# Kernel tuning notes

Hardware: AMD Instinct MI355X
Metric: run time of the kernel (lower is better)

Reference implementation:

```python
import jax, jax.numpy as jnp
import numpy as np


def setup_inputs() -> dict:
    key = jax.random.key(0)
    ks = jax.random.split(key, 10)
    B, T = 256, 256
    num_q, dk, dv, C = 1000, 128, 128, 32
    xn_k = (2.0 / (dk + C)) ** 0.5   # xavier_normal for Mk
    xn_v = (2.0 / (C + dv)) ** 0.5   # xavier_normal for Mv
    return dict(
        skills=jax.random.randint(ks[0], (B, T), 0, num_q),
        responses=jax.random.randint(ks[1], (B, T), 0, 2),
        k_emb=jax.random.normal(ks[2], (num_q, dk), dtype=jnp.float32) * 0.05,
        v_emb=jax.random.normal(ks[3], (2 * num_q, dv), dtype=jnp.float32) * 0.05,
        Mk=jax.random.normal(ks[4], (dk, C), dtype=jnp.float32) * xn_k,
        Mv0=jax.random.normal(ks[5], (C, dv), dtype=jnp.float32) * xn_v,
        f_W=jax.random.normal(ks[6], (2 * dk, dk), dtype=jnp.float32) * 0.05,
        f_b=jnp.zeros((dk,), jnp.float32),
        p_W=jax.random.normal(ks[7], (dk, 1), dtype=jnp.float32) * 0.05,
        p_b=jnp.zeros((1,), jnp.float32),
        e_W=jax.random.normal(ks[8], (dv, dv), dtype=jnp.float32) * 0.05,
        e_b=jnp.zeros((dv,), jnp.float32),
        a_W=jax.random.normal(ks[9], (dv, dv), dtype=jnp.float32) * 0.05,
        a_b=jnp.zeros((dv,), jnp.float32),
    )


def reference(skills, responses, k_emb, v_emb, Mk, Mv0, f_W, f_b,
              p_W, p_b, e_W, e_b, a_W, a_b):
    num_q = k_emb.shape[0]
    B = skills.shape[0]
    masked_r = responses * (responses > -1).astype(responses.dtype)
    qr = skills + num_q * masked_r
    kt_all = k_emb[skills]   # (B, T, dk)
    vt_all = v_emb[qr]       # (B, T, dv)
    Mvt0 = jnp.broadcast_to(Mv0[None], (B,) + Mv0.shape)  # (B, C, dv)

    def step(Mvt, xs):
        kt, vt = xs                                      # (B,dk), (B,dv)
        wt = jax.nn.softmax(kt @ Mk, axis=-1)            # (B, C) read weights
        rt = jnp.einsum('bc,bcd->bd', wt, Mvt)           # memory read
        ft = jnp.tanh(jnp.concatenate([rt, kt], axis=-1) @ f_W + f_b)
        pt = jax.nn.sigmoid(ft @ p_W + p_b)[:, 0]        # (B,)
        et = jax.nn.sigmoid(vt @ e_W + e_b)              # erase gate
        at = jnp.tanh(vt @ a_W + a_b)                    # add vector
        Mvt = Mvt * (1.0 - wt[:, :, None] * et[:, None, :]) \
              + wt[:, :, None] * at[:, None, :]
        return Mvt, pt

    xs = (jnp.swapaxes(kt_all, 0, 1), jnp.swapaxes(vt_all, 0, 1))  # time-major
    _, p = jax.lax.scan(step, Mvt0, xs)                  # (T, B)
    p = jnp.swapaxes(p, 0, 1)                            # (B, T)
    pred = p[:, :-1]
    true = responses[:, 1:].astype(jnp.float32)
    return pred, true
```

## Files before the change

kernel.cpp:

```cpp
#include <hip/hip_runtime.h>
#include <math.h>

#define BB 256
#define TT 256
#define NQ 1000
#define DK 128
#define DV 128
#define CC 32

typedef short s16x8 __attribute__((ext_vector_type(8)));
typedef float f32x4 __attribute__((ext_vector_type(4)));
typedef float f32x2 __attribute__((ext_vector_type(2)));

__device__ __forceinline__ float fast_sigmoid(float x) {
    x = fminf(fmaxf(x, -30.f), 30.f);
    return 1.f / (1.f + __expf(-x));
}
__device__ __forceinline__ float fast_tanh(float x) {
    x = fminf(fmaxf(x, -15.f), 15.f);
    float t = __expf(2.f * x);
    return (t - 1.f) / (t + 1.f);
}
__device__ __forceinline__ unsigned short f2bf(float f) {
    unsigned u = __float_as_uint(f);
    u += 0x7fffu + ((u >> 16) & 1u);
    return (unsigned short)(u >> 16);
}
__device__ __forceinline__ float bf2f(unsigned short h) {
    return __uint_as_float((unsigned)h << 16);
}
__device__ __forceinline__ unsigned u4get(uint4 v, int i) {
    return i == 0 ? v.x : i == 1 ? v.y : i == 2 ? v.z : v.w;
}
__device__ __forceinline__ f32x2 mk2(float x, float y) { f32x2 r; r.x = x; r.y = y; return r; }
__device__ __forceinline__ f32x2 fma2(f32x2 a, f32x2 b, f32x2 c) {
    return __builtin_elementwise_fma(a, b, c);
}
__device__ __forceinline__ s16x8 cvt8(float4 v0, float4 v1) {
    s16x8 f;
    f[0] = (short)f2bf(v0.x); f[1] = (short)f2bf(v0.y);
    f[2] = (short)f2bf(v0.z); f[3] = (short)f2bf(v0.w);
    f[4] = (short)f2bf(v1.x); f[5] = (short)f2bf(v1.y);
    f[6] = (short)f2bf(v1.z); f[7] = (short)f2bf(v1.w);
    return f;
}

__global__ __launch_bounds__(256) void conv_kernel(
    const float* __restrict__ eW, const float* __restrict__ aW,
    const float* __restrict__ fW, const float* __restrict__ Mk,
    unsigned short* __restrict__ eWt, unsigned short* __restrict__ aWt,
    unsigned short* __restrict__ fWat, unsigned short* __restrict__ fWbt,
    unsigned short* __restrict__ Mkt)
{
    int idx = blockIdx.x * 256 + threadIdx.x;
    if (idx < 16384) {
        int n = idx >> 7, k = idx & 127;
        eWt[idx] = f2bf(eW[k * 128 + n]);
    } else if (idx < 32768) {
        int i = idx - 16384; int n = i >> 7, k = i & 127;
        aWt[i] = f2bf(aW[k * 128 + n]);
    } else if (idx < 49152) {
        int i = idx - 32768; int n = i >> 7, k = i & 127;
        fWat[i] = f2bf(fW[k * 128 + n]);
    } else if (idx < 65536) {
        int i = idx - 49152; int n = i >> 7, k = i & 127;
        fWbt[i] = f2bf(fW[(128 + k) * 128 + n]);
    } else if (idx < 69632) {
        int i = idx - 65536; int n = i >> 7, k = i & 127;
        Mkt[i] = f2bf(Mk[k * 32 + n]);
    }
}

__global__ __launch_bounds__(256) void pre_kernel(
    const int* __restrict__ skills, const int* __restrict__ responses,
    const float* __restrict__ k_emb, const float* __restrict__ v_emb,
    const float* __restrict__ fb, const float* __restrict__ eb,
    const float* __restrict__ ab,
    const unsigned short* __restrict__ Mkt, const unsigned short* __restrict__ fWbt,
    const unsigned short* __restrict__ eWt, const unsigned short* __restrict__ aWt,
    float* __restrict__ Wo, unsigned* __restrict__ EA,
    unsigned short* __restrict__ Ko, float* __restrict__ outTrue,
    int t0, int Tc)
{
    const int tid = threadIdx.x;
    const int lane = tid & 63;
    const int m_base = (tid >> 6) * 16;
    const int mrow = lane & 15, quad = lane >> 4;
    const size_t base = (size_t)blockIdx.x * 64;

    __shared__ __align__(16) unsigned short Wlds[128 * 136];

    int grow = (int)base + m_base + mrow;
    int gb = grow / Tc;
    int gt = t0 + (grow - gb * Tc);
    int gi = gb * TT + gt;
    int s = skills[gi];
    int r = responses[gi];
    int q = s + NQ * ((r > -1) ? r : 0);
    if (quad == 0 && gt >= 1) outTrue[gb * (TT - 1) + (gt - 1)] = (float)r;

    {
        int n = tid >> 3, k0 = (tid & 7) * 16;
        *(s16x8*)&Wlds[n * 136 + k0]     = *(const s16x8*)&Mkt[n * 128 + k0];
        *(s16x8*)&Wlds[n * 136 + k0 + 8] = *(const s16x8*)&Mkt[n * 128 + k0 + 8];
    }

    s16x8 aF[4];
    {
        const float* kr = k_emb + (size_t)s * DK + quad * 8;
#pragma unroll
        for (int kb = 0; kb < 4; ++kb)
            aF[kb] = cvt8(*(const float4*)(kr + kb * 32),
                          *(const float4*)(kr + kb * 32 + 4));
    }
    __syncthreads();

    {
        f32x4 l0 = {0.f, 0.f, 0.f, 0.f}, l1 = {0.f, 0.f, 0.f, 0.f};
#pragma unroll
        for (int kb = 0; kb < 4; ++kb) {
            s16x8 b0 = *(const s16x8*)&Wlds[mrow * 136 + kb * 32 + quad * 8];
            s16x8 b1 = *(const s16x8*)&Wlds[(16 + mrow) * 136 + kb * 32 + quad * 8];
            l0 = __builtin_amdgcn_mfma_f32_16x16x32_bf16(aF[kb], b0, l0, 0, 0, 0);
            l1 = __builtin_amdgcn_mfma_f32_16x16x32_bf16(aF[kb], b1, l1, 0, 0, 0);
        }
#pragma unroll
        for (int reg = 0; reg < 4; ++reg) {
            float a0 = l0[reg], a1 = l1[reg];
            float m = fmaxf(a0, a1);
#pragma unroll
            for (int off = 1; off < 16; off <<= 1)
                m = fmaxf(m, __shfl_xor(m, off, 64));
            float e0 = __expf(a0 - m), e1 = __expf(a1 - m);
            float ssum = e0 + e1;
#pragma unroll
            for (int off = 1; off < 16; off <<= 1)
                ssum += __shfl_xor(ssum, off, 64);
            float inv = 1.f / ssum;
            size_t rowg = base + m_base + quad * 4 + reg;
            Wo[rowg * 32 + mrow]      = e0 * inv;
            Wo[rowg * 32 + 16 + mrow] = e1 * inv;
        }
    }
    __syncthreads();

    {
        int n = tid >> 1, k0 = (tid & 1) * 64;
#pragma unroll
        for (int j = 0; j < 8; ++j)
            *(s16x8*)&Wlds[n * 136 + k0 + j * 8] = *(const s16x8*)&fWbt[n * 128 + k0 + j * 8];
    }
    __syncthreads();

    s16x8 vF[4];
    {
        const float* vr = v_emb + (size_t)q * DV + quad * 8;
#pragma unroll
        for (int kb = 0; kb < 4; ++kb)
            vF[kb] = cvt8(*(const float4*)(vr + kb * 32),
                          *(const float4*)(vr + kb * 32 + 4));
    }

#pragma unroll
    for (int nt = 0; nt < 8; ++nt) {
        f32x4 acc = {0.f, 0.f, 0.f, 0.f};
#pragma unroll
        for (int kb = 0; kb < 4; ++kb) {
            s16x8 bf = *(const s16x8*)&Wlds[(nt * 16 + mrow) * 136 + kb * 32 + quad * 8];
            acc = __builtin_amdgcn_mfma_f32_16x16x32_bf16(aF[kb], bf, acc, 0, 0, 0);
        }
        int col = nt * 16 + mrow;
        float fbv = fb[col];
#pragma unroll
        for (int reg = 0; reg < 4; ++reg) {
            size_t rr = base + m_base + quad * 4 + reg;
            Ko[rr * 128 + col] = f2bf(acc[reg] + fbv);
        }
    }
    __syncthreads();

    {
        int n = tid >> 1, k0 = (tid & 1) * 64;
#pragma unroll
        for (int j = 0; j < 8; ++j)
            *(s16x8*)&Wlds[n * 136 + k0 + j * 8] = *(const s16x8*)&eWt[n * 128 + k0 + j * 8];
    }
    __syncthreads();

    float etr[8][4];
#pragma unroll
    for (int nt = 0; nt < 8; ++nt) {
        f32x4 acc = {0.f, 0.f, 0.f, 0.f};
#pragma unroll
        for (int kb = 0; kb < 4; ++kb) {
            s16x8 bf = *(const s16x8*)&Wlds[(nt * 16 + mrow) * 136 + kb * 32 + quad * 8];
            acc = __builtin_amdgcn_mfma_f32_16x16x32_bf16(vF[kb], bf, acc, 0, 0, 0);
        }
        int col = nt * 16 + mrow;
        float ebv = eb[col];
#pragma unroll
        for (int reg = 0; reg < 4; ++reg)
            etr[nt][reg] = fast_sigmoid(acc[reg] + ebv);
    }
    __syncthreads();

    {
        int n = tid >> 1, k0 = (tid & 1) * 64;
#pragma unroll
        for (int j = 0; j < 8; ++j)
            *(s16x8*)&Wlds[n * 136 + k0 + j * 8] = *(const s16x8*)&aWt[n * 128 + k0 + j * 8];
    }
    __syncthreads();

#pragma unroll
    for (int nt = 0; nt < 8; ++nt) {
        f32x4 acc = {0.f, 0.f, 0.f, 0.f};
#pragma unroll
        for (int kb = 0; kb < 4; ++kb) {
            s16x8 bf = *(const s16x8*)&Wlds[(nt * 16 + mrow) * 136 + kb * 32 + quad * 8];
            acc = __builtin_amdgcn_mfma_f32_16x16x32_bf16(vF[kb], bf, acc, 0, 0, 0);
        }
        int col = nt * 16 + mrow;
        float abv = ab[col];
#pragma unroll
        for (int reg = 0; reg < 4; ++reg) {
            size_t rr = base + m_base + quad * 4 + reg;
            int bb = (int)(rr / (size_t)Tc);
            int t  = (int)(rr - (size_t)bb * Tc);
            size_t o4 = (((size_t)bb * (Tc >> 5) + (t >> 5)) * 8 + ((t >> 2) & 7)) * 128 + col;
            unsigned lo = f2bf(etr[nt][reg]);
            unsigned hi = (unsigned)f2bf(fast_tanh(acc[reg] + abv)) << 16;
            EA[o4 * 4 + (t & 3)] = hi | lo;
        }
    }
}


#define CH 32
#define WROW 36
#define RSTR 136
#define PSTR 132
#define SB() __builtin_amdgcn_sched_barrier(0)

#define LOAD_W(gg) do {                                                       \
    const float* ws = Wb + (size_t)(gg) * CH * 32;                            \
    wr0 = *(const float4*)(ws + dd * 8);                                      \
    wr1 = *(const float4*)(ws + dd * 8 + 4);                                  \
} while (0)

#define PUB_W(gg) do {                                                        \
    float* wd = &Wl[(gg) & 1][lr * WROW + lq * 8];                            \
    *(float4*)wd = wr0; *(float4*)(wd + 4) = wr1;                             \
} while (0)

#define LOAD_EA(ER, gg) do {                                                  \
    const uint4* src = EA4 + ((size_t)(bq + (gg))) * 1024 + dd;               \
    _Pragma("unroll")                                                         \
    for (int j = 0; j < 8; ++j) ER[j] = src[j * 128];                         \
} while (0)

#define PREF4(A0,A1,A2,A3, rowidx) do {                                       \
    const float* _wr = wlc + (rowidx) * WROW;                                 \
    A0 = *(const float4*)(_wr + 0);  A1 = *(const float4*)(_wr + 4);          \
    A2 = *(const float4*)(_wr + 8);  A3 = *(const float4*)(_wr + 12);         \
} while (0)

#define STEP4(A0,A1,A2,A3, ER, tl) do {                                       \
    f32x2 w2[8];                                                              \
    w2[0] = mk2(A0.x, A0.y); w2[1] = mk2(A0.z, A0.w);                         \
    w2[2] = mk2(A1.x, A1.y); w2[3] = mk2(A1.z, A1.w);                         \
    w2[4] = mk2(A2.x, A2.y); w2[5] = mk2(A2.z, A2.w);                         \
    w2[6] = mk2(A3.x, A3.y); w2[7] = mk2(A3.z, A3.w);                         \
    unsigned ea = u4get(ER[(tl) >> 2], (tl) & 3);                             \
    float e  = __uint_as_float(ea << 16);                                     \
    float av = __uint_as_float(ea & 0xffff0000u);                             \
    f32x2 ne2 = mk2(-e, -e);                                                  \
    f32x2 a2  = mk2(av, av);                                                  \
    f32x2 r0 = mk2(0.f, 0.f), r1 = r0, r2 = r0, r3 = r0;                      \
    r0 = fma2(w2[0], Mv2[0], r0); r1 = fma2(w2[1], Mv2[1], r1);               \
    r2 = fma2(w2[2], Mv2[2], r2); r3 = fma2(w2[3], Mv2[3], r3);               \
    r0 = fma2(w2[4], Mv2[4], r0); r1 = fma2(w2[5], Mv2[5], r1);               \
    r2 = fma2(w2[6], Mv2[6], r2); r3 = fma2(w2[7], Mv2[7], r3);               \
    f32x2 rs = (r0 + r1) + (r2 + r3);                                         \
    slp[(tl) * PSTR + dd] = rs.x + rs.y;                                      \
    _Pragma("unroll")                                                         \
    for (int i = 0; i < 8; ++i)                                               \
        Mv2[i] = fma2(w2[i], fma2(ne2, Mv2[i], a2), Mv2[i]);                  \
} while (0)

#define SEQ_CHUNK4(ER, gg) do {                                               \
    const float* wlc = Wl[(gg) & 1] + ch16;                                   \
    float* slp = ch ? &rt1[(gg) & 1][0] : &rt0[(gg) & 1][0];                  \
    PREF4(w0, w1, w2_, w3_, 0);                                               \
    PREF4(u0, u1, u2, u3, 1);                                                 \
    _Pragma("unroll")                                                         \
    for (int tp = 0; tp < 8; ++tp) {                                          \
        SB(); PREF4(v0, v1, v2, v3, 4 * tp + 2); SB();                        \
        STEP4(w0, w1, w2_, w3_, ER, 4 * tp);                                  \
        SB(); PREF4(x0, x1, x2, x3, 4 * tp + 3); SB();                        \
        STEP4(u0, u1, u2, u3, ER, 4 * tp + 1);                                \
        SB(); PREF4(w0, w1, w2_, w3_,                                         \
                    (4 * tp + 4 < 32) ? (4 * tp + 4) : 31); SB();             \
        STEP4(v0, v1, v2, v3, ER, 4 * tp + 2);                                \
        SB(); PREF4(u0, u1, u2, u3,                                           \
                    (4 * tp + 5 < 32) ? (4 * tp + 5) : 31); SB();             \
        STEP4(x0, x1, x2, x3, ER, 4 * tp + 3);                                \
    }                                                                         \
} while (0)

__device__ __forceinline__ void consume_chunk(
    int gc, const float* r0p, const float* r1p, const unsigned short* fWl,
    int b, int Tc, int t0,
    const unsigned short* __restrict__ Ko, const float* __restrict__ pW,
    float pbv, float* __restrict__ pred, int tid)
{
    const int lane = tid & 63;
    const int cw = (tid >> 6) & 1;
    const int mrow = lane & 15, quad = lane >> 4;
    s16x8 aF[4];
#pragma unroll
    for (int kb = 0; kb < 4; ++kb) {
        const float* s0 = r0p + (cw * 16 + mrow) * PSTR + kb * 32 + quad * 8;
        const float* s1 = r1p + (cw * 16 + mrow) * PSTR + kb * 32 + quad * 8;
        float4 xa = *(const float4*)s0, xb = *(const float4*)(s0 + 4);
        float4 ya = *(const float4*)s1, yb = *(const float4*)(s1 + 4);
        float4 sa, sb;
        sa.x = xa.x + ya.x; sa.y = xa.y + ya.y; sa.z = xa.z + ya.z; sa.w = xa.w + ya.w;
        sb.x = xb.x + yb.x; sb.y = xb.y + yb.y; sb.z = xb.z + yb.z; sb.w = xb.w + yb.w;
        aF[kb] = cvt8(sa, sb);
    }
    float p0 = 0.f, p1 = 0.f, p2 = 0.f, p3 = 0.f;
    size_t rbase = (size_t)b * Tc + gc * CH + cw * 16 + quad * 4;
#pragma unroll
    for (int nt = 0; nt < 8; ++nt) {
        f32x4 acc = {0.f, 0.f, 0.f, 0.f};
#pragma unroll
        for (int kb = 0; kb < 4; ++kb) {
            s16x8 bf = *(const s16x8*)&fWl[(nt * 16 + mrow) * RSTR + kb * 32 + quad * 8];
            acc = __builtin_amdgcn_mfma_f32_16x16x32_bf16(aF[kb], bf, acc, 0, 0, 0);
        }
        int col = nt * 16 + mrow;
        float pw = pW[col];
        p0 = fmaf(fast_tanh(acc[0] + bf2f(Ko[(rbase + 0) * 128 + col])), pw, p0);
        p1 = fmaf(fast_tanh(acc[1] + bf2f(Ko[(rbase + 1) * 128 + col])), pw, p1);
        p2 = fmaf(fast_tanh(acc[2] + bf2f(Ko[(rbase + 2) * 128 + col])), pw, p2);
        p3 = fmaf(fast_tanh(acc[3] + bf2f(Ko[(rbase + 3) * 128 + col])), pw, p3);
    }
#pragma unroll
    for (int off = 1; off < 16; off <<= 1) {
        p0 += __shfl_xor(p0, off, 64); p1 += __shfl_xor(p1, off, 64);
        p2 += __shfl_xor(p2, off, 64); p3 += __shfl_xor(p3, off, 64);
    }
    if (mrow == 0) {
        int tb = t0 + gc * CH + cw * 16 + quad * 4;
        float ps[4] = {p0, p1, p2, p3};
#pragma unroll
        for (int reg = 0; reg < 4; ++reg) {
            int t = tb + reg;
            if (t < TT - 1) pred[b * (TT - 1) + t] = fast_sigmoid(ps[reg] + pbv);
        }
    }
}

__global__ __launch_bounds__(512, 1) void fused_kernel(
    const float* __restrict__ W, const unsigned* __restrict__ EA,
    const float* __restrict__ Mv0, const unsigned short* __restrict__ Ko,
    const unsigned short* __restrict__ fWat, const float* __restrict__ pW,
    const float* __restrict__ pb,
    float* __restrict__ pred, float* __restrict__ MvWS,
    int t0, int Tc, int doInit, int doSave)
{
    const int b = blockIdx.x;
    const int tid = threadIdx.x;
    const int nch = Tc / CH;
    const int role = tid >> 7;
    const int dd = tid & 127;
    const int ch = role & 1;
    const int ch16 = ch * 16;

    __shared__ __align__(16) float Wl[2][CH * WROW];
    __shared__ __align__(16) float rt0[2][CH * PSTR];
    __shared__ __align__(16) float rt1[2][CH * PSTR];
    __shared__ __align__(16) unsigned short fWl[128 * RSTR];

    {
        int n = tid >> 2, k0 = (tid & 3) * 32;
#pragma unroll
        for (int j = 0; j < 4; ++j)
            *(s16x8*)&fWl[n * RSTR + k0 + j * 8] = *(const s16x8*)&fWat[n * 128 + k0 + j * 8];
    }

    const int lr = dd >> 2, lq = tid & 3;
    const float* __restrict__ Wb = W + (size_t)b * Tc * 32;
    const uint4* __restrict__ EA4 = (const uint4*)EA;
    const int bq = b * nch;
    f32x2 Mv2[8];
    float4 wr0, wr1;
    float4 w0, w1, w2_, w3_;
    float4 u0, u1, u2, u3;
    float4 v0, v1, v2, v3;
    float4 x0, x1, x2, x3;
    uint4 erA[8], erB[8];
    float pbv = 0.f;

    if (role < 2) {
        if (doInit) {
#pragma unroll
            for (int i = 0; i < 8; ++i)
                Mv2[i] = mk2(Mv0[(ch16 + 2 * i) * 128 + dd],
                             Mv0[(ch16 + 2 * i + 1) * 128 + dd]);
        } else {
#pragma unroll
            for (int i = 0; i < 8; ++i)
                Mv2[i] = mk2(MvWS[(size_t)b * 4096 + (ch16 + 2 * i) * 128 + dd],
                             MvWS[(size_t)b * 4096 + (ch16 + 2 * i + 1) * 128 + dd]);
        }
        LOAD_EA(erA, 0);
    } else if (role == 3) {
        LOAD_W(0); PUB_W(0);
        if (nch > 1) LOAD_W(1);
    } else {
        pbv = pb[0];
    }
    __syncthreads();

    for (int g = 0; g < nch; g += 2) {
        if (role < 2) {
            if (g + 1 < nch) LOAD_EA(erB, g + 1);
            SEQ_CHUNK4(erA, g);
        } else if (role == 2) {
            if (g >= 1)
                consume_chunk(g - 1, &rt0[(g - 1) & 1][0], &rt1[(g - 1) & 1][0],
                              fWl, b, Tc, t0, Ko, pW, pbv, pred, tid);
        } else {
            if (g + 1 < nch) PUB_W(g + 1);
            if (g + 2 < nch) LOAD_W(g + 2);
        }
        __syncthreads();

        if (role < 2) {
            if (g + 1 < nch) {
                if (g + 2 < nch) LOAD_EA(erA, g + 2);
                SEQ_CHUNK4(erB, g + 1);
            }
        } else if (role == 2) {
            consume_chunk(g, &rt0[g & 1][0], &rt1[g & 1][0],
                          fWl, b, Tc, t0, Ko, pW, pbv, pred, tid);
        } else {
            if (g + 2 < nch) PUB_W(g + 2);
            if (g + 3 < nch) LOAD_W(g + 3);
        }
        __syncthreads();
    }
    if (!(nch & 1) && role == 2) {
        consume_chunk(nch - 1, &rt0[(nch - 1) & 1][0], &rt1[(nch - 1) & 1][0],
                      fWl, b, Tc, t0, Ko, pW, pbv, pred, tid);
    }

    if (doSave && role < 2) {
#pragma unroll
        for (int i = 0; i < 8; ++i) {
            MvWS[(size_t)b * 4096 + (ch16 + 2 * i) * 128 + dd]     = Mv2[i].x;
            MvWS[(size_t)b * 4096 + (ch16 + 2 * i + 1) * 128 + dd] = Mv2[i].y;
        }
    }
}


extern "C" void kernel_launch(void* const* d_in, const int* in_sizes, int n_in,
                              void* d_out, int out_size, void* d_ws, size_t ws_size,
                              hipStream_t stream) {
    const int*   skills    = (const int*)d_in[0];
    const int*   responses = (const int*)d_in[1];
    const float* k_emb     = (const float*)d_in[2];
    const float* v_emb     = (const float*)d_in[3];
    const float* Mk        = (const float*)d_in[4];
    const float* Mv0       = (const float*)d_in[5];
    const float* f_W       = (const float*)d_in[6];
    const float* f_b       = (const float*)d_in[7];
    const float* p_W       = (const float*)d_in[8];
    const float* p_b       = (const float*)d_in[9];
    const float* e_W       = (const float*)d_in[10];
    const float* e_b       = (const float*)d_in[11];
    const float* a_W       = (const float*)d_in[12];
    const float* a_b       = (const float*)d_in[13];

    float* pred    = (float*)d_out;
    float* outTrue = pred + BB * (TT - 1);

    int Tc = TT;
    for (;;) {
        size_t need = (size_t)BB * Tc * 896 + 69632 * 2;
        if (Tc < TT) need += (size_t)BB * 4096 * 4;
        if (need <= ws_size || Tc <= 32) break;
        Tc >>= 1;
    }

    char* p = (char*)d_ws;
    float* Wo = (float*)p;                     p += (size_t)BB * Tc * 32 * 4;
    unsigned* EA = (unsigned*)p;               p += (size_t)BB * Tc * 128 * 4;
    unsigned short* Ko = (unsigned short*)p;   p += (size_t)BB * Tc * 128 * 2;
    unsigned short* eWt = (unsigned short*)p;  p += 16384 * 2;
    unsigned short* aWt = (unsigned short*)p;  p += 16384 * 2;
    unsigned short* fWat = (unsigned short*)p; p += 16384 * 2;
    unsigned short* fWbt = (unsigned short*)p; p += 16384 * 2;
    unsigned short* Mkt = (unsigned short*)p;  p += 4096 * 2;
    float* MvWS = (float*)p;

    conv_kernel<<<272, 256, 0, stream>>>(e_W, a_W, f_W, Mk,
                                         eWt, aWt, fWat, fWbt, Mkt);

    for (int t0 = 0; t0 < TT; t0 += Tc) {
        pre_kernel<<<(BB * Tc) / 64, 256, 0, stream>>>(
            skills, responses, k_emb, v_emb, f_b, e_b, a_b,
            Mkt, fWbt, eWt, aWt, Wo, EA, Ko, outTrue, t0, Tc);
        fused_kernel<<<BB, 512, 0, stream>>>(
            Wo, EA, Mv0, Ko, fWat, p_W, p_b, pred, MvWS,
            t0, Tc, t0 == 0 ? 1 : 0, (t0 + Tc < TT) ? 1 : 0);
    }
}
```

Measured before the change: 157.5 us.

## Split memory-update recurrence across four lanes per column with shuffle-reduced reads

The sequential memory update is spread over 512 threads instead of 256. Each thread now holds 8 memory slots for one value column, not 16, and the four lanes of a column combine their partial read sums with cross-lane shuffles. This shortens the per-timestep serial FMA chain and removes the second read buffer and the add that merged the two halves in the consumer. The cost is a 768-thread block, two shuffles per step, and each EA vector being loaded redundantly by four lanes.

```diff
diff --git a/kernel.cpp b/kernel.cpp
--- a/kernel.cpp
+++ b/kernel.cpp
@@ -244,8 +244,8 @@
 
 #define LOAD_W(gg) do {                                                       \
     const float* ws = Wb + (size_t)(gg) * CH * 32;                            \
-    wr0 = *(const float4*)(ws + dd * 8);                                      \
-    wr1 = *(const float4*)(ws + dd * 8 + 4);                                  \
+    wr0 = *(const float4*)(ws + sd * 8);                                      \
+    wr1 = *(const float4*)(ws + sd * 8 + 4);                                  \
 } while (0)
 
 #define PUB_W(gg) do {                                                        \
@@ -259,57 +259,53 @@
     for (int j = 0; j < 8; ++j) ER[j] = src[j * 128];                         \
 } while (0)
 
-#define PREF4(A0,A1,A2,A3, rowidx) do {                                       \
+#define PREF2(A0,A1, rowidx) do {                                             \
     const float* _wr = wlc + (rowidx) * WROW;                                 \
     A0 = *(const float4*)(_wr + 0);  A1 = *(const float4*)(_wr + 4);          \
-    A2 = *(const float4*)(_wr + 8);  A3 = *(const float4*)(_wr + 12);         \
 } while (0)
 
-#define STEP4(A0,A1,A2,A3, ER, tl) do {                                       \
-    f32x2 w2[8];                                                              \
+#define STEP2(A0,A1, ER, tl) do {                                             \
+    f32x2 w2[4];                                                              \
     w2[0] = mk2(A0.x, A0.y); w2[1] = mk2(A0.z, A0.w);                         \
     w2[2] = mk2(A1.x, A1.y); w2[3] = mk2(A1.z, A1.w);                         \
-    w2[4] = mk2(A2.x, A2.y); w2[5] = mk2(A2.z, A2.w);                         \
-    w2[6] = mk2(A3.x, A3.y); w2[7] = mk2(A3.z, A3.w);                         \
     unsigned ea = u4get(ER[(tl) >> 2], (tl) & 3);                             \
     float e  = __uint_as_float(ea << 16);                                     \
     float av = __uint_as_float(ea & 0xffff0000u);                             \
     f32x2 ne2 = mk2(-e, -e);                                                  \
     f32x2 a2  = mk2(av, av);                                                  \
-    f32x2 r0 = mk2(0.f, 0.f), r1 = r0, r2 = r0, r3 = r0;                      \
+    f32x2 r0 = mk2(0.f, 0.f), r1 = r0;                                        \
     r0 = fma2(w2[0], Mv2[0], r0); r1 = fma2(w2[1], Mv2[1], r1);               \
-    r2 = fma2(w2[2], Mv2[2], r2); r3 = fma2(w2[3], Mv2[3], r3);               \
-    r0 = fma2(w2[4], Mv2[4], r0); r1 = fma2(w2[5], Mv2[5], r1);               \
-    r2 = fma2(w2[6], Mv2[6], r2); r3 = fma2(w2[7], Mv2[7], r3);               \
-    f32x2 rs = (r0 + r1) + (r2 + r3);                                         \
-    slp[(tl) * PSTR + dd] = rs.x + rs.y;                                      \
+    r0 = fma2(w2[2], Mv2[2], r0); r1 = fma2(w2[3], Mv2[3], r1);               \
+    f32x2 rs = r0 + r1;                                                       \
+    float sum = rs.x + rs.y;                                                  \
+    sum += __shfl_xor(sum, 1, 64);                                            \
+    sum += __shfl_xor(sum, 2, 64);                                            \
+    if (cq == 0) slp[(tl) * PSTR + dd] = sum;                                 \
     _Pragma("unroll")                                                         \
-    for (int i = 0; i < 8; ++i)                                               \
+    for (int i = 0; i < 4; ++i)                                               \
         Mv2[i] = fma2(w2[i], fma2(ne2, Mv2[i], a2), Mv2[i]);                  \
 } while (0)
 
-#define SEQ_CHUNK4(ER, gg) do {                                               \
-    const float* wlc = Wl[(gg) & 1] + ch16;                                   \
-    float* slp = ch ? &rt1[(gg) & 1][0] : &rt0[(gg) & 1][0];                  \
-    PREF4(w0, w1, w2_, w3_, 0);                                               \
-    PREF4(u0, u1, u2, u3, 1);                                                 \
+#define SEQ_CHUNK2(ER, gg) do {                                               \
+    const float* wlc = Wl[(gg) & 1] + cq * 8;                                 \
+    float* slp = &rt[(gg) & 1][0];                                            \
+    PREF2(w0, w1, 0);                                                         \
+    PREF2(u0, u1, 1);                                                         \
     _Pragma("unroll")                                                         \
     for (int tp = 0; tp < 8; ++tp) {                                          \
-        SB(); PREF4(v0, v1, v2, v3, 4 * tp + 2); SB();                        \
-        STEP4(w0, w1, w2_, w3_, ER, 4 * tp);                                  \
-        SB(); PREF4(x0, x1, x2, x3, 4 * tp + 3); SB();                        \
-        STEP4(u0, u1, u2, u3, ER, 4 * tp + 1);                                \
-        SB(); PREF4(w0, w1, w2_, w3_,                                         \
-                    (4 * tp + 4 < 32) ? (4 * tp + 4) : 31); SB();             \
-        STEP4(v0, v1, v2, v3, ER, 4 * tp + 2);                                \
-        SB(); PREF4(u0, u1, u2, u3,                                           \
-                    (4 * tp + 5 < 32) ? (4 * tp + 5) : 31); SB();             \
-        STEP4(x0, x1, x2, x3, ER, 4 * tp + 3);                                \
+        SB(); PREF2(v0, v1, 4 * tp + 2); SB();                                \
+        STEP2(w0, w1, ER, 4 * tp);                                            \
+        SB(); PREF2(x0, x1, 4 * tp + 3); SB();                                \
+        STEP2(u0, u1, ER, 4 * tp + 1);                                        \
+        SB(); PREF2(w0, w1, (4 * tp + 4 < 32) ? (4 * tp + 4) : 31); SB();     \
+        STEP2(v0, v1, ER, 4 * tp + 2);                                        \
+        SB(); PREF2(u0, u1, (4 * tp + 5 < 32) ? (4 * tp + 5) : 31); SB();     \
+        STEP2(x0, x1, ER, 4 * tp + 3);                                        \
     }                                                                         \
 } while (0)
 
 __device__ __forceinline__ void consume_chunk(
-    int gc, const float* r0p, const float* r1p, const unsigned short* fWl,
+    int gc, const float* rp, const unsigned short* fWl,
     int b, int Tc, int t0,
     const unsigned short* __restrict__ Ko, const float* __restrict__ pW,
     float pbv, float* __restrict__ pred, int tid)
@@ -320,14 +316,8 @@
     s16x8 aF[4];
 #pragma unroll
     for (int kb = 0; kb < 4; ++kb) {
-        const float* s0 = r0p + (cw * 16 + mrow) * PSTR + kb * 32 + quad * 8;
-        const float* s1 = r1p + (cw * 16 + mrow) * PSTR + kb * 32 + quad * 8;
-        float4 xa = *(const float4*)s0, xb = *(const float4*)(s0 + 4);
-        float4 ya = *(const float4*)s1, yb = *(const float4*)(s1 + 4);
-        float4 sa, sb;
-        sa.x = xa.x + ya.x; sa.y = xa.y + ya.y; sa.z = xa.z + ya.z; sa.w = xa.w + ya.w;
-        sb.x = xb.x + yb.x; sb.y = xb.y + yb.y; sb.z = xb.z + yb.z; sb.w = xb.w + yb.w;
-        aF[kb] = cvt8(sa, sb);
+        const float* s0 = rp + (cw * 16 + mrow) * PSTR + kb * 32 + quad * 8;
+        aF[kb] = cvt8(*(const float4*)s0, *(const float4*)(s0 + 4));
     }
     float p0 = 0.f, p1 = 0.f, p2 = 0.f, p3 = 0.f;
     size_t rbase = (size_t)b * Tc + gc * CH + cw * 16 + quad * 4;
@@ -362,7 +352,7 @@
     }
 }
 
-__global__ __launch_bounds__(512, 1) void fused_kernel(
+__global__ __launch_bounds__(768, 1) void fused_kernel(
     const float* __restrict__ W, const unsigned* __restrict__ EA,
     const float* __restrict__ Mv0, const unsigned short* __restrict__ Ko,
     const unsigned short* __restrict__ fWat, const float* __restrict__ pW,
@@ -374,49 +364,45 @@
     const int tid = threadIdx.x;
     const int nch = Tc / CH;
     const int role = tid >> 7;
-    const int dd = tid & 127;
-    const int ch = role & 1;
-    const int ch16 = ch * 16;
+    const int dd = tid >> 2;
+    const int cq = tid & 3;
+    const int sd = tid & 127;
 
     __shared__ __align__(16) float Wl[2][CH * WROW];
-    __shared__ __align__(16) float rt0[2][CH * PSTR];
-    __shared__ __align__(16) float rt1[2][CH * PSTR];
+    __shared__ __align__(16) float rt[2][CH * PSTR];
     __shared__ __align__(16) unsigned short fWl[128 * RSTR];
 
-    {
+    if (tid < 512) {
         int n = tid >> 2, k0 = (tid & 3) * 32;
 #pragma unroll
         for (int j = 0; j < 4; ++j)
             *(s16x8*)&fWl[n * RSTR + k0 + j * 8] = *(const s16x8*)&fWat[n * 128 + k0 + j * 8];
     }
 
-    const int lr = dd >> 2, lq = tid & 3;
+    const int lr = sd >> 2, lq = tid & 3;
     const float* __restrict__ Wb = W + (size_t)b * Tc * 32;
     const uint4* __restrict__ EA4 = (const uint4*)EA;
     const int bq = b * nch;
-    f32x2 Mv2[8];
+    f32x2 Mv2[4];
     float4 wr0, wr1;
-    float4 w0, w1, w2_, w3_;
-    float4 u0, u1, u2, u3;
-    float4 v0, v1, v2, v3;
-    float4 x0, x1, x2, x3;
+    float4 w0, w1, u0, u1, v0, v1, x0, x1;
     uint4 erA[8], erB[8];
     float pbv = 0.f;
 
-    if (role < 2) {
+    if (role < 4) {
         if (doInit) {
 #pragma unroll
-            for (int i = 0; i < 8; ++i)
-                Mv2[i] = mk2(Mv0[(ch16 + 2 * i) * 128 + dd],
-                             Mv0[(ch16 + 2 * i + 1) * 128 + dd]);
+            for (int i = 0; i < 4; ++i)
+                Mv2[i] = mk2(Mv0[(cq * 8 + 2 * i) * 128 + dd],
+                             Mv0[(cq * 8 + 2 * i + 1) * 128 + dd]);
         } else {
 #pragma unroll
-            for (int i = 0; i < 8; ++i)
-                Mv2[i] = mk2(MvWS[(size_t)b * 4096 + (ch16 + 2 * i) * 128 + dd],
-                             MvWS[(size_t)b * 4096 + (ch16 + 2 * i + 1) * 128 + dd]);
+            for (int i = 0; i < 4; ++i)
+                Mv2[i] = mk2(MvWS[(size_t)b * 4096 + (cq * 8 + 2 * i) * 128 + dd],
+                             MvWS[(size_t)b * 4096 + (cq * 8 + 2 * i + 1) * 128 + dd]);
         }
         LOAD_EA(erA, 0);
-    } else if (role == 3) {
+    } else if (role == 5) {
         LOAD_W(0); PUB_W(0);
         if (nch > 1) LOAD_W(1);
     } else {
@@ -425,43 +411,43 @@
     __syncthreads();
 
     for (int g = 0; g < nch; g += 2) {
-        if (role < 2) {
+        if (role < 4) {
             if (g + 1 < nch) LOAD_EA(erB, g + 1);
-            SEQ_CHUNK4(erA, g);
-        } else if (role == 2) {
+            SEQ_CHUNK2(erA, g);
+        } else if (role == 4) {
             if (g >= 1)
-                consume_chunk(g - 1, &rt0[(g - 1) & 1][0], &rt1[(g - 1) & 1][0],
-                              fWl, b, Tc, t0, Ko, pW, pbv, pred, tid);
+                consume_chunk(g - 1, &rt[(g - 1) & 1][0], fWl,
+                              b, Tc, t0, Ko, pW, pbv, pred, tid);
         } else {
             if (g + 1 < nch) PUB_W(g + 1);
             if (g + 2 < nch) LOAD_W(g + 2);
         }
         __syncthreads();
 
-        if (role < 2) {
+        if (role < 4) {
             if (g + 1 < nch) {
                 if (g + 2 < nch) LOAD_EA(erA, g + 2);
-                SEQ_CHUNK4(erB, g + 1);
+                SEQ_CHUNK2(erB, g + 1);
             }
-        } else if (role == 2) {
-            consume_chunk(g, &rt0[g & 1][0], &rt1[g & 1][0],
-                          fWl, b, Tc, t0, Ko, pW, pbv, pred, tid);
+        } else if (role == 4) {
+            consume_chunk(g, &rt[g & 1][0], fWl,
+                          b, Tc, t0, Ko, pW, pbv, pred, tid);
         } else {
             if (g + 2 < nch) PUB_W(g + 2);
             if (g + 3 < nch) LOAD_W(g + 3);
         }
         __syncthreads();
     }
-    if (!(nch & 1) && role == 2) {
-        consume_chunk(nch - 1, &rt0[(nch - 1) & 1][0], &rt1[(nch - 1) & 1][0],
-                      fWl, b, Tc, t0, Ko, pW, pbv, pred, tid);
-    }
-
-    if (doSave && role < 2) {
-#pragma unroll
-        for (int i = 0; i < 8; ++i) {
-            MvWS[(size_t)b * 4096 + (ch16 + 2 * i) * 128 + dd]     = Mv2[i].x;
-            MvWS[(size_t)b * 4096 + (ch16 + 2 * i + 1) * 128 + dd] = Mv2[i].y;
+    if (!(nch & 1) && role == 4) {
+        consume_chunk(nch - 1, &rt[(nch - 1) & 1][0], fWl,
+                      b, Tc, t0, Ko, pW, pbv, pred, tid);
+    }
+
+    if (doSave && role < 4) {
+#pragma unroll
+        for (int i = 0; i < 4; ++i) {
+            MvWS[(size_t)b * 4096 + (cq * 8 + 2 * i) * 128 + dd]     = Mv2[i].x;
+            MvWS[(size_t)b * 4096 + (cq * 8 + 2 * i + 1) * 128 + dd] = Mv2[i].y;
         }
     }
 }
@@ -514,7 +500,7 @@
         pre_kernel<<<(BB * Tc) / 64, 256, 0, stream>>>(
             skills, responses, k_emb, v_emb, f_b, e_b, a_b,
             Mkt, fWbt, eWt, aWt, Wo, EA, Ko, outTrue, t0, Tc);
-        fused_kernel<<<BB, 512, 0, stream>>>(
+        fused_kernel<<<BB, 768, 0, stream>>>(
             Wo, EA, Mv0, Ko, fWat, p_W, p_b, pred, MvWS,
             t0, Tc, t0 == 0 ? 1 : 0, (t0 + Tc < TT) ? 1 : 0);
     }
```

Measured after the change: 165.9 us. 1.05x slower.

## Stage erase/add vectors through LDS by loader warps instead of per-thread registers

Applied to the files above, without the earlier changes.

The recurrence warps no longer hold the packed erase/add data for the next chunk in 16 uint4 registers. Instead, role-3 warps load it from global memory and publish it into a new double-buffered LDS array, alongside the read-weight tiles. The sequential loop shrinks its prefetch depth from 4 to 2 row groups and reads one erase/add word per step from LDS. The aim is to cut register pressure and global-load latency on the critical recurrence path, at the cost of extra LDS traffic and shared-memory footprint.

```diff
diff --git a/kernel.cpp b/kernel.cpp
--- a/kernel.cpp
+++ b/kernel.cpp
@@ -28,9 +28,6 @@
 }
 __device__ __forceinline__ float bf2f(unsigned short h) {
     return __uint_as_float((unsigned)h << 16);
-}
-__device__ __forceinline__ unsigned u4get(uint4 v, int i) {
-    return i == 0 ? v.x : i == 1 ? v.y : i == 2 ? v.z : v.w;
 }
 __device__ __forceinline__ f32x2 mk2(float x, float y) { f32x2 r; r.x = x; r.y = y; return r; }
 __device__ __forceinline__ f32x2 fma2(f32x2 a, f32x2 b, f32x2 c) {
@@ -253,10 +250,17 @@
     *(float4*)wd = wr0; *(float4*)(wd + 4) = wr1;                             \
 } while (0)
 
-#define LOAD_EA(ER, gg) do {                                                  \
+#define STAGE_EA(gg) do {                                                     \
     const uint4* src = EA4 + ((size_t)(bq + (gg))) * 1024 + dd;               \
+    unsigned* dst = &EAl[(gg) & 1][0];                                        \
     _Pragma("unroll")                                                         \
-    for (int j = 0; j < 8; ++j) ER[j] = src[j * 128];                         \
+    for (int j = 0; j < 8; ++j) {                                             \
+        uint4 v = src[j * 128];                                               \
+        dst[(4 * j + 0) * 128 + dd] = v.x;                                    \
+        dst[(4 * j + 1) * 128 + dd] = v.y;                                    \
+        dst[(4 * j + 2) * 128 + dd] = v.z;                                    \
+        dst[(4 * j + 3) * 128 + dd] = v.w;                                    \
+    }                                                                         \
 } while (0)
 
 #define PREF4(A0,A1,A2,A3, rowidx) do {                                       \
@@ -265,13 +269,13 @@
     A2 = *(const float4*)(_wr + 8);  A3 = *(const float4*)(_wr + 12);         \
 } while (0)
 
-#define STEP4(A0,A1,A2,A3, ER, tl) do {                                       \
+#define STEP4(A0,A1,A2,A3, EAV, tl) do {                                      \
     f32x2 w2[8];                                                              \
     w2[0] = mk2(A0.x, A0.y); w2[1] = mk2(A0.z, A0.w);                         \
     w2[2] = mk2(A1.x, A1.y); w2[3] = mk2(A1.z, A1.w);                         \
     w2[4] = mk2(A2.x, A2.y); w2[5] = mk2(A2.z, A2.w);                         \
     w2[6] = mk2(A3.x, A3.y); w2[7] = mk2(A3.z, A3.w);                         \
-    unsigned ea = u4get(ER[(tl) >> 2], (tl) & 3);                             \
+    unsigned ea = (EAV);                                                      \
     float e  = __uint_as_float(ea << 16);                                     \
     float av = __uint_as_float(ea & 0xffff0000u);                             \
     f32x2 ne2 = mk2(-e, -e);                                                  \
@@ -288,23 +292,21 @@
         Mv2[i] = fma2(w2[i], fma2(ne2, Mv2[i], a2), Mv2[i]);                  \
 } while (0)
 
-#define SEQ_CHUNK4(ER, gg) do {                                               \
+#define SEQ_CHUNK4(gg) do {                                                   \
     const float* wlc = Wl[(gg) & 1] + ch16;                                   \
+    const unsigned* eac = &EAl[(gg) & 1][0];                                  \
     float* slp = ch ? &rt1[(gg) & 1][0] : &rt0[(gg) & 1][0];                  \
     PREF4(w0, w1, w2_, w3_, 0);                                               \
-    PREF4(u0, u1, u2, u3, 1);                                                 \
+    unsigned eaw = eac[dd], eau;                                              \
     _Pragma("unroll")                                                         \
-    for (int tp = 0; tp < 8; ++tp) {                                          \
-        SB(); PREF4(v0, v1, v2, v3, 4 * tp + 2); SB();                        \
-        STEP4(w0, w1, w2_, w3_, ER, 4 * tp);                                  \
-        SB(); PREF4(x0, x1, x2, x3, 4 * tp + 3); SB();                        \
-        STEP4(u0, u1, u2, u3, ER, 4 * tp + 1);                                \
+    for (int tp = 0; tp < 16; ++tp) {                                         \
+        SB(); PREF4(u0, u1, u2, u3, 2 * tp + 1);                              \
+        eau = eac[(2 * tp + 1) * 128 + dd]; SB();                             \
+        STEP4(w0, w1, w2_, w3_, eaw, 2 * tp);                                 \
         SB(); PREF4(w0, w1, w2_, w3_,                                         \
-                    (4 * tp + 4 < 32) ? (4 * tp + 4) : 31); SB();             \
-        STEP4(v0, v1, v2, v3, ER, 4 * tp + 2);                                \
-        SB(); PREF4(u0, u1, u2, u3,                                           \
-                    (4 * tp + 5 < 32) ? (4 * tp + 5) : 31); SB();             \
-        STEP4(x0, x1, x2, x3, ER, 4 * tp + 3);                                \
+                    (2 * tp + 2 < 32) ? (2 * tp + 2) : 31);                   \
+        eaw = eac[((2 * tp + 2 < 32) ? (2 * tp + 2) : 31) * 128 + dd]; SB();  \
+        STEP4(u0, u1, u2, u3, eau, 2 * tp + 1);                               \
     }                                                                         \
 } while (0)
 
@@ -381,6 +383,7 @@
     __shared__ __align__(16) float Wl[2][CH * WROW];
     __shared__ __align__(16) float rt0[2][CH * PSTR];
     __shared__ __align__(16) float rt1[2][CH * PSTR];
+    __shared__ __align__(16) unsigned EAl[2][CH * 128];
     __shared__ __align__(16) unsigned short fWl[128 * RSTR];
 
     {
@@ -398,9 +401,6 @@
     float4 wr0, wr1;
     float4 w0, w1, w2_, w3_;
     float4 u0, u1, u2, u3;
-    float4 v0, v1, v2, v3;
-    float4 x0, x1, x2, x3;
-    uint4 erA[8], erB[8];
     float pbv = 0.f;
 
     if (role < 2) {
@@ -415,10 +415,10 @@
                 Mv2[i] = mk2(MvWS[(size_t)b * 4096 + (ch16 + 2 * i) * 128 + dd],
                              MvWS[(size_t)b * 4096 + (ch16 + 2 * i + 1) * 128 + dd]);
         }
-        LOAD_EA(erA, 0);
     } else if (role == 3) {
         LOAD_W(0); PUB_W(0);
         if (nch > 1) LOAD_W(1);
+        STAGE_EA(0);
     } else {
         pbv = pb[0];
     }
@@ -426,28 +426,24 @@
 
     for (int g = 0; g < nch; g += 2) {
         if (role < 2) {
-            if (g + 1 < nch) LOAD_EA(erB, g + 1);
-            SEQ_CHUNK4(erA, g);
+            SEQ_CHUNK4(g);
         } else if (role == 2) {
             if (g >= 1)
                 consume_chunk(g - 1, &rt0[(g - 1) & 1][0], &rt1[(g - 1) & 1][0],
                               fWl, b, Tc, t0, Ko, pW, pbv, pred, tid);
         } else {
-            if (g + 1 < nch) PUB_W(g + 1);
+            if (g + 1 < nch) { PUB_W(g + 1); STAGE_EA(g + 1); }
             if (g + 2 < nch) LOAD_W(g + 2);
         }
         __syncthreads();
 
         if (role < 2) {
-            if (g + 1 < nch) {
-                if (g + 2 < nch) LOAD_EA(erA, g + 2);
-                SEQ_CHUNK4(erB, g + 1);
-            }
+            if (g + 1 < nch) SEQ_CHUNK4(g + 1);
         } else if (role == 2) {
             consume_chunk(g, &rt0[g & 1][0], &rt1[g & 1][0],
                           fWl, b, Tc, t0, Ko, pW, pbv, pred, tid);
         } else {
-            if (g + 2 < nch) PUB_W(g + 2);
+            if (g + 2 < nch) { PUB_W(g + 2); STAGE_EA(g + 2); }
             if (g + 3 < nch) LOAD_W(g + 3);
         }
         __syncthreads();
```

Result: no change. 155.4 us (median of 2 runs) (-1.4%).
